# Kernel optimization log

Measured on AMD Instinct MI355X. Metric: run time of the kernel, lower is better.

## Reference

```python
import math
import jax, jax.numpy as jnp
import numpy as np

B, T, D = 8, 2048, 256
N_TICKS, DT, P_MIN, P_MAX = 3, 1.0, 2.0, 4.0


def setup_inputs() -> dict:
    key = jax.random.key(0)
    ks = jax.random.split(key, 16)
    s = 1.0 / math.sqrt(D)
    w = lambda k: jax.random.normal(k, (D, D), jnp.float32) * s
    zb = jnp.zeros((D,), jnp.float32)
    return {
        "z": jax.random.normal(ks[0], (B, T, D), jnp.float32),
        "in_w": w(ks[1]), "in_b": zb,
        "ln_g": jnp.ones((D,), jnp.float32), "ln_b": zb,
        "q_w": w(ks[2]), "q_b": zb,
        "k_w": w(ks[3]), "k_b": zb,
        "v_w": w(ks[4]), "v_b": zb,
        "o_w": w(ks[5]), "o_b": zb,
        "log_tau": jnp.zeros((D,), jnp.float32),
        "p1_w": w(ks[6]), "p1_b": zb,
        "p2_w": w(ks[7]), "p2_b": zb,
    }


def _layernorm(x, g, b, eps=1e-5):
    mu = jnp.mean(x, axis=-1, keepdims=True)
    var = jnp.var(x, axis=-1, keepdims=True)
    return (x - mu) * jax.lax.rsqrt(var + eps) * g + b


def _lin(x, w, b):
    return x @ w.T + b


def reference(z, in_w, in_b, ln_g, ln_b, q_w, q_b, k_w, k_b, v_w, v_b,
              o_w, o_b, log_tau, p1_w, p1_b, p2_w, p2_b):
    tau = jnp.exp(log_tau)  # [d]
    inv_sqrt_d = 1.0 / math.sqrt(D)
    uniform = 1.0 / T
    pred_losses, eff_ps = [], []
    for _ in range(N_TICKS):
        h = _layernorm(_lin(z, in_w, in_b), ln_g, ln_b)
        Q, K, V = _lin(h, q_w, q_b), _lin(h, k_w, k_b), _lin(h, v_w, v_b)
        sim = jnp.einsum('btd,bsd->bts', Q, K) * inv_sqrt_d  # [B,T,T]
        attn = jax.nn.softmax(sim, axis=-1)
        row_max = jnp.max(attn, axis=-1)  # [B,T]
        conf = (jnp.mean(row_max, axis=-1) - uniform) / (1.0 - uniform + 1e-6)
        conf = jnp.clip(conf, 0.0, 1.0)  # [B]
        eff_p = P_MIN + (P_MAX - P_MIN) * conf
        eff_ps.append(jax.lax.stop_gradient(eff_p))
        attn_sharp = jax.nn.softmax(sim * eff_p[:, None, None], axis=-1)
        context = jnp.einsum('bts,bsd->btd', attn_sharp, V)
        target = _lin(context, o_w, o_b)
        z_pred = _lin(jax.nn.relu(_lin(z, p1_w, p1_b)), p2_w, p2_b)
        dz = (target - z) / (tau + 1e-6)
        z_next = z + DT * dz
        pred_losses.append(jnp.mean((z_pred - jax.lax.stop_gradient(z_next)) ** 2))
        z = z_next
    pred_loss_mean = jnp.mean(jnp.stack(pred_losses))
    eff_p_mean = jnp.mean(jnp.concatenate(eff_ps))
    return z, pred_loss_mean, eff_p_mean
```

## Files before the change

kernel.cpp:

```cpp
#include <hip/hip_runtime.h>
#include <math.h>

#define Bn 8
#define Tn 2048
#define Dn 256
#define NTICK 3
#define NROWS (Bn*Tn)
#define ABM 64
#define NBLKA (NROWS/ABM)
#define BS 64
#define GM 64
#define NBLKG (NROWS/GM)
#define WP 65536

typedef unsigned int u32;
typedef unsigned short u16;
typedef __attribute__((ext_vector_type(8))) short bf16x8;
typedef __attribute__((ext_vector_type(4))) float f32x4;
typedef __attribute__((ext_vector_type(16))) float f32x16;

__device__ __forceinline__ float bf2f(u32 u){
  union { u32 i; float f; } x; x.i = u << 16; return x.f;
}
__device__ __forceinline__ u16 f2bf(float f){
  union { float f; u32 i; } x; x.f = f;
  u32 r = (x.i + 0x7fffu + ((x.i >> 16) & 1u)) >> 16;
  return (u16)r;
}
__device__ __forceinline__ void gld_lds16(const u16* gsrc, u16* ldst){
  __builtin_amdgcn_global_load_lds(
      (const __attribute__((address_space(1))) u32*)(const void*)gsrc,
      (__attribute__((address_space(3))) u32*)(void*)ldst, 16, 0, 0);
}

__device__ __forceinline__ void stage_A(const u16* __restrict__ A, int row0, char* smem){
  const int tid = threadIdx.x, lane = tid & 63, w = tid >> 6;
  #pragma unroll
  for (int r=0;r<8;++r){
    int s = w*16 + 2*r + (lane>>5);
    int slot = (lane & 31) ^ (s & 7);
    gld_lds16(A + (size_t)(row0 + s)*Dn + slot*8, (u16*)(smem + (w*16 + 2*r)*512));
  }
}
__device__ __forceinline__ void load_frags(const char* smem, bf16x8* af){
  const int tid = threadIdx.x, lane = tid & 63, w = tid >> 6;
  const int l7 = lane & 7, g = (lane >> 4) & 3, q15 = lane & 15;
  const char* ab = smem + (w*16 + q15)*512;
  #pragma unroll
  for (int kk=0;kk<8;++kk) af[kk] = *(const bf16x8*)(ab + 16*((4*kk+g)^l7));
}
__device__ __forceinline__ void stage_Wchunk(const u16* __restrict__ W, int c, char* wbuf){
  const int tid = threadIdx.x, lane = tid & 63, w = tid >> 6;
  #pragma unroll
  for (int r=0;r<2;++r){
    int rl = w*4 + 2*r + (lane>>5);
    int slot = (lane & 31) ^ (rl & 7);
    gld_lds16(W + (size_t)(c*16 + rl)*Dn + slot*8, (u16*)(wbuf + (w*4 + 2*r)*512));
  }
}
__device__ __forceinline__ void load_wfrags(const char* wbuf, bf16x8* wf){
  const int lane = threadIdx.x & 63;
  const int l7 = lane & 7, g = (lane >> 4) & 3, q15 = lane & 15;
  const char* wb_ = wbuf + q15*512;
  #pragma unroll
  for (int kk=0;kk<8;++kk) wf[kk] = *(const bf16x8*)(wb_ + 16*((4*kk+g)^l7));
}
__device__ __forceinline__ void zero_acc(f32x4* acc){
  #pragma unroll
  for (int nt=0;nt<16;++nt) acc[nt] = (f32x4){0.f,0.f,0.f,0.f};
}
#define CHUNK_STEP(c, NC, PLANE_OF, IDX_OF)                                    \
  asm volatile("s_waitcnt lgkmcnt(0)" ::: "memory");                           \
  if ((c) < (NC)-2) { asm volatile("s_waitcnt vmcnt(2)" ::: "memory"); }       \
  else              { asm volatile("s_waitcnt vmcnt(0)" ::: "memory"); }       \
  __builtin_amdgcn_sched_barrier(0);                                           \
  __builtin_amdgcn_s_barrier();                                                \
  if ((c)+3 < (NC)) stage_Wchunk(PLANE_OF((c)+3), IDX_OF((c)+3), ring + (((c)+3)&3)*8192);

__global__ void k_prep(const float* __restrict__ s0, const float* __restrict__ s1,
                       const float* __restrict__ s2, const float* __restrict__ s3,
                       const float* __restrict__ s4, const float* __restrict__ s5,
                       const float* __restrict__ s6, u16* __restrict__ dst){
  int y = blockIdx.y;
  const float* s = (y==0)?s0:(y==1)?s1:(y==2)?s2:(y==3)?s3:(y==4)?s4:(y==5)?s5:s6;
  int i = (blockIdx.x*256 + threadIdx.x)*4;
  float4 v = *(const float4*)(s + i);
  u16 h0=f2bf(v.x), h1=f2bf(v.y), h2=f2bf(v.z), h3=f2bf(v.w);
  uint2 hi, lo;
  hi.x = (u32)h0 | ((u32)h1 << 16);
  hi.y = (u32)h2 | ((u32)h3 << 16);
  lo.x = (u32)f2bf(v.x - bf2f(h0)) | ((u32)f2bf(v.y - bf2f(h1)) << 16);
  lo.y = (u32)f2bf(v.z - bf2f(h2)) | ((u32)f2bf(v.w - bf2f(h3)) << 16);
  *(uint2*)(dst + (size_t)y*WP + i) = hi;
  *(uint2*)(dst + (size_t)(7+y)*WP + i) = lo;
}

__global__ void k_split(const float* __restrict__ s, u16* __restrict__ dh, u16* __restrict__ dl,
                        float* __restrict__ stats){
  if (blockIdx.x == 0 && threadIdx.x < 64) stats[threadIdx.x] = 0.f;
  int i = (blockIdx.x*256 + threadIdx.x)*4;
  float4 v = *(const float4*)(s + i);
  u16 h0=f2bf(v.x), h1=f2bf(v.y), h2=f2bf(v.z), h3=f2bf(v.w);
  uint2 hi, lo;
  hi.x = (u32)h0 | ((u32)h1 << 16);
  hi.y = (u32)h2 | ((u32)h3 << 16);
  lo.x = (u32)f2bf(v.x - bf2f(h0)) | ((u32)f2bf(v.y - bf2f(h1)) << 16);
  lo.y = (u32)f2bf(v.z - bf2f(h2)) | ((u32)f2bf(v.w - bf2f(h3)) << 16);
  *(uint2*)(dh + i) = hi;
  *(uint2*)(dl + i) = lo;
}

__global__ __launch_bounds__(256) void k_gemm_ln(
    const u16* __restrict__ Ahi, const u16* __restrict__ Alo,
    const u16* __restrict__ Whi, const u16* __restrict__ Wlo,
    const float* __restrict__ bias, const float* __restrict__ gamma, const float* __restrict__ beta,
    u16* __restrict__ h)
{
  __shared__ __align__(16) char smem[65536];
  char* ring = smem;
  f32x4 acc[16];
  const int row0 = blockIdx.x * GM;
  stage_A(Ahi, row0, smem);
  stage_A(Alo, row0, smem + 32768);
  asm volatile("s_waitcnt vmcnt(0)" ::: "memory");
  __builtin_amdgcn_sched_barrier(0);
  bf16x8 afh[8], afl[8];
  load_frags(smem, afh);
  load_frags(smem + 32768, afl);
  asm volatile("s_waitcnt lgkmcnt(0)" ::: "memory");
  __builtin_amdgcn_sched_barrier(0);
  __builtin_amdgcn_s_barrier();
  zero_acc(acc);
  #define LN_PL(i) ((i) < 16 ? Whi : Wlo)
  #define LN_IX(i) ((i) & 15)
  stage_Wchunk(LN_PL(0), LN_IX(0), ring + 0*8192);
  stage_Wchunk(LN_PL(1), LN_IX(1), ring + 1*8192);
  stage_Wchunk(LN_PL(2), LN_IX(2), ring + 2*8192);
  asm volatile("s_waitcnt vmcnt(4)" ::: "memory");
  __builtin_amdgcn_sched_barrier(0);
  __builtin_amdgcn_s_barrier();
  for (int c=0; c<32; ++c){
    bf16x8 wf[8];
    load_wfrags(ring + (c&3)*8192, wf);
    int nt = c & 15;
    if (c < 16){
      #pragma unroll
      for (int kk=0;kk<8;++kk)
        acc[nt] = __builtin_amdgcn_mfma_f32_16x16x32_bf16(afh[kk], wf[kk], acc[nt], 0,0,0);
      #pragma unroll
      for (int kk=0;kk<8;++kk)
        acc[nt] = __builtin_amdgcn_mfma_f32_16x16x32_bf16(afl[kk], wf[kk], acc[nt], 0,0,0);
    } else {
      #pragma unroll
      for (int kk=0;kk<8;++kk)
        acc[nt] = __builtin_amdgcn_mfma_f32_16x16x32_bf16(afh[kk], wf[kk], acc[nt], 0,0,0);
    }
    CHUNK_STEP(c, 32, LN_PL, LN_IX)
  }
  const int tid = threadIdx.x, lane = tid & 63, w = tid >> 6;
  const int g4 = lane >> 4, q15 = lane & 15;
  float bcol[16], gcol[16], becol[16];
  #pragma unroll
  for (int nt=0;nt<16;++nt){
    int col = nt*16 + q15;
    bcol[nt] = bias[col]; gcol[nt] = gamma[col]; becol[nt] = beta[col];
  }
  float mu[4], rstd[4];
  #pragma unroll
  for (int j=0;j<4;++j){
    float s=0.f, q=0.f;
    #pragma unroll
    for (int nt=0;nt<16;++nt){ float v = acc[nt][j] + bcol[nt]; s += v; q += v*v; }
    #pragma unroll
    for (int off=1; off<16; off<<=1){ s += __shfl_xor(s,off); q += __shfl_xor(q,off); }
    float m = s*(1.f/Dn);
    mu[j] = m; rstd[j] = rsqrtf(q*(1.f/Dn) - m*m + 1e-5f);
  }
  const size_t rbase = (size_t)(row0 + w*16 + g4*4);
  #pragma unroll
  for (int nt=0;nt<16;++nt){
    #pragma unroll
    for (int j=0;j<4;++j){
      float v = (acc[nt][j] + bcol[nt] - mu[j])*rstd[j]*gcol[nt] + becol[nt];
      h[(rbase+j)*Dn + nt*16 + q15] = f2bf(v);
    }
  }
}

__global__ __launch_bounds__(256) void k_gemm_qkv(
    const u16* __restrict__ h, const u16* __restrict__ wbf,
    const float* __restrict__ qb, const float* __restrict__ kb, const float* __restrict__ vb,
    u16* __restrict__ Qo, u16* __restrict__ Ko, u16* __restrict__ Vo)
{
  __shared__ __align__(16) char smem[65536];
  char* ring = smem + 32768;
  f32x4 acc[16];
  const int row0 = blockIdx.x * GM;
  stage_A(h, row0, smem);
  #define QKV_PL(i) (wbf + ((size_t)((((i)>>5)+1) + (((i)>>4)&1)*7))*WP)
  #define QKV_IX(i) ((i) & 15)
  stage_Wchunk(QKV_PL(0), QKV_IX(0), ring + 0*8192);
  stage_Wchunk(QKV_PL(1), QKV_IX(1), ring + 1*8192);
  stage_Wchunk(QKV_PL(2), QKV_IX(2), ring + 2*8192);
  asm volatile("s_waitcnt vmcnt(4)" ::: "memory");
  __builtin_amdgcn_sched_barrier(0);
  bf16x8 af[8];
  load_frags(smem, af);
  zero_acc(acc);
  const int tid = threadIdx.x, lane = tid & 63, w = tid >> 6;
  const int g4 = lane >> 4, q15 = lane & 15;
  const size_t rbase = (size_t)(row0 + w*16 + g4*4);
  __builtin_amdgcn_s_barrier();
  for (int c=0; c<96; ++c){
    bf16x8 wf[8];
    load_wfrags(ring + (c&3)*8192, wf);
    int nt = c & 15;
    #pragma unroll
    for (int kk=0;kk<8;++kk)
      acc[nt] = __builtin_amdgcn_mfma_f32_16x16x32_bf16(af[kk], wf[kk], acc[nt], 0,0,0);
    CHUNK_STEP(c, 96, QKV_PL, QKV_IX)
    if ((c & 31) == 31){
      int p = c >> 5;
      const float* bias = (p==0) ? qb : (p==1) ? kb : vb;
      u16* out = (p==0) ? Qo : (p==1) ? Ko : Vo;
      #pragma unroll
      for (int nt2=0;nt2<16;++nt2){
        float bc = bias[nt2*16 + q15];
        #pragma unroll
        for (int j=0;j<4;++j)
          out[(rbase+j)*Dn + nt2*16 + q15] = f2bf(acc[nt2][j] + bc);
      }
      zero_acc(acc);
    }
  }
}

__global__ __launch_bounds__(256) void k_gemm_update(
    const u16* __restrict__ Chi, const u16* __restrict__ Clo,
    const u16* __restrict__ Whi, const u16* __restrict__ Wlo,
    const float* __restrict__ ob,
    const u16* __restrict__ zhi_old, const u16* __restrict__ zlo_old,
    const float* __restrict__ log_tau,
    u16* __restrict__ zhi_new, u16* __restrict__ zlo_new,
    float* __restrict__ zout)
{
  __shared__ __align__(16) char smem[65536];
  char* ring = smem;
  f32x4 acc[16];
  const int row0 = blockIdx.x * GM;
  stage_A(Chi, row0, smem);
  stage_A(Clo, row0, smem + 32768);
  asm volatile("s_waitcnt vmcnt(0)" ::: "memory");
  __builtin_amdgcn_sched_barrier(0);
  bf16x8 afh[8], afl[8];
  load_frags(smem, afh);
  load_frags(smem + 32768, afl);
  asm volatile("s_waitcnt lgkmcnt(0)" ::: "memory");
  __builtin_amdgcn_sched_barrier(0);
  __builtin_amdgcn_s_barrier();
  zero_acc(acc);
  stage_Wchunk(LN_PL(0), LN_IX(0), ring + 0*8192);
  stage_Wchunk(LN_PL(1), LN_IX(1), ring + 1*8192);
  stage_Wchunk(LN_PL(2), LN_IX(2), ring + 2*8192);
  asm volatile("s_waitcnt vmcnt(4)" ::: "memory");
  __builtin_amdgcn_sched_barrier(0);
  __builtin_amdgcn_s_barrier();
  for (int c=0; c<32; ++c){
    bf16x8 wf[8];
    load_wfrags(ring + (c&3)*8192, wf);
    int nt = c & 15;
    if (c < 16){
      #pragma unroll
      for (int kk=0;kk<8;++kk)
        acc[nt] = __builtin_amdgcn_mfma_f32_16x16x32_bf16(afh[kk], wf[kk], acc[nt], 0,0,0);
      #pragma unroll
      for (int kk=0;kk<8;++kk)
        acc[nt] = __builtin_amdgcn_mfma_f32_16x16x32_bf16(afl[kk], wf[kk], acc[nt], 0,0,0);
    } else {
      #pragma unroll
      for (int kk=0;kk<8;++kk)
        acc[nt] = __builtin_amdgcn_mfma_f32_16x16x32_bf16(afh[kk], wf[kk], acc[nt], 0,0,0);
    }
    CHUNK_STEP(c, 32, LN_PL, LN_IX)
  }
  const int tid = threadIdx.x, lane = tid & 63, w = tid >> 6;
  const int g4 = lane >> 4, q15 = lane & 15;
  const size_t rbase = (size_t)(row0 + w*16 + g4*4);
  #pragma unroll
  for (int nt=0;nt<16;++nt){
    int col = nt*16 + q15;
    float bc = ob[col];
    float invt = 1.f/(expf(log_tau[col]) + 1e-6f);
    #pragma unroll
    for (int j=0;j<4;++j){
      size_t idx = (rbase+j)*Dn + col;
      float zo = bf2f(zhi_old[idx]) + bf2f(zlo_old[idx]);
      float zn = zo + (acc[nt][j] + bc - zo)*invt;
      u16 zh = f2bf(zn);
      zhi_new[idx] = zh;
      zlo_new[idx] = f2bf(zn - bf2f(zh));
      if (zout) zout[idx] = zn;
    }
  }
}

__global__ __launch_bounds__(256) void k_gemm_relu(
    const u16* __restrict__ A, const u16* __restrict__ Wb, const float* __restrict__ bias,
    u16* __restrict__ t1)
{
  __shared__ __align__(16) char smem[65536];
  char* ring = smem + 32768;
  f32x4 acc[16];
  const int row0 = blockIdx.x * GM;
  stage_A(A, row0, smem);
  #define W1_PL(i) (Wb)
  #define W1_IX(i) (i)
  stage_Wchunk(Wb, 0, ring + 0*8192);
  stage_Wchunk(Wb, 1, ring + 1*8192);
  stage_Wchunk(Wb, 2, ring + 2*8192);
  asm volatile("s_waitcnt vmcnt(4)" ::: "memory");
  __builtin_amdgcn_sched_barrier(0);
  bf16x8 af[8];
  load_frags(smem, af);
  zero_acc(acc);
  __builtin_amdgcn_s_barrier();
  for (int c=0; c<16; ++c){
    bf16x8 wf[8];
    load_wfrags(ring + (c&3)*8192, wf);
    #pragma unroll
    for (int kk=0;kk<8;++kk)
      acc[c] = __builtin_amdgcn_mfma_f32_16x16x32_bf16(af[kk], wf[kk], acc[c], 0,0,0);
    CHUNK_STEP(c, 16, W1_PL, W1_IX)
  }
  const int tid = threadIdx.x, lane = tid & 63, w = tid >> 6;
  const int g4 = lane >> 4, q15 = lane & 15;
  const size_t rbase = (size_t)(row0 + w*16 + g4*4);
  #pragma unroll
  for (int nt=0;nt<16;++nt){
    float bc = bias[nt*16 + q15];
    #pragma unroll
    for (int j=0;j<4;++j)
      t1[(rbase+j)*Dn + nt*16 + q15] = f2bf(fmaxf(acc[nt][j] + bc, 0.f));
  }
}

__global__ __launch_bounds__(256) void k_gemm_loss(
    const u16* __restrict__ t1, const u16* __restrict__ Wb, const float* __restrict__ bias,
    const u16* __restrict__ zhi_new, const u16* __restrict__ zlo_new,
    float* __restrict__ loss_acc)
{
  __shared__ __align__(16) char smem[65536];
  __shared__ float red[4];
  char* ring = smem + 32768;
  f32x4 acc[16];
  const int row0 = blockIdx.x * GM;
  stage_A(t1, row0, smem);
  stage_Wchunk(Wb, 0, ring + 0*8192);
  stage_Wchunk(Wb, 1, ring + 1*8192);
  stage_Wchunk(Wb, 2, ring + 2*8192);
  asm volatile("s_waitcnt vmcnt(4)" ::: "memory");
  __builtin_amdgcn_sched_barrier(0);
  bf16x8 af[8];
  load_frags(smem, af);
  zero_acc(acc);
  __builtin_amdgcn_s_barrier();
  for (int c=0; c<16; ++c){
    bf16x8 wf[8];
    load_wfrags(ring + (c&3)*8192, wf);
    #pragma unroll
    for (int kk=0;kk<8;++kk)
      acc[c] = __builtin_amdgcn_mfma_f32_16x16x32_bf16(af[kk], wf[kk], acc[c], 0,0,0);
    CHUNK_STEP(c, 16, W1_PL, W1_IX)
  }
  const int tid = threadIdx.x, lane = tid & 63, w = tid >> 6;
  const int g4 = lane >> 4, q15 = lane & 15;
  const size_t rbase = (size_t)(row0 + w*16 + g4*4);
  float lsum = 0.f;
  #pragma unroll
  for (int nt=0;nt<16;++nt){
    float bc = bias[nt*16 + q15];
    #pragma unroll
    for (int j=0;j<4;++j){
      size_t idx = (rbase+j)*Dn + nt*16 + q15;
      float zn = bf2f(zhi_new[idx]) + bf2f(zlo_new[idx]);
      float dn = acc[nt][j] + bc - zn;
      lsum += dn*dn;
    }
  }
  #pragma unroll
  for (int off=1; off<64; off<<=1) lsum += __shfl_xor(lsum, off);
  if (lane == 0) red[w] = lsum;
  __syncthreads();
  if (tid == 0) atomicAdd(loss_acc, red[0]+red[1]+red[2]+red[3]);
}

__global__ __launch_bounds__(256) void k_passA(
    const u16* __restrict__ Qg, const u16* __restrict__ Kg,
    float* __restrict__ conf_b)
{
  __shared__ __align__(16) char smem[65536];
  const int tid = threadIdx.x;
  const int lane = tid & 63, w = tid >> 6;
  const int l31 = lane & 31, hi5 = lane >> 5;
  const int qh = w >> 1, sh = w & 1;
  const int row0 = blockIdx.x * ABM;
  const int b = row0 >> 11;
  const size_t kbase = (size_t)b * Tn * Dn;

  #pragma unroll
  for (int r=0;r<8;++r){
    int s = w*16 + 2*r + (lane>>5);
    int slot = (lane & 31) ^ (s & 7);
    gld_lds16(Qg + (size_t)(row0 + s)*Dn + slot*8, (u16*)(smem + (w*16 + 2*r)*512));
  }
  asm volatile("s_waitcnt vmcnt(0)" ::: "memory");
  __builtin_amdgcn_sched_barrier(0);
  __builtin_amdgcn_s_barrier();
  bf16x8 qf[16];
  {
    const char* qb = smem + (qh*32 + l31)*512;
    const int r7 = l31 & 7;
    #pragma unroll
    for (int t=0;t<16;++t) qf[t] = *(const bf16x8*)(qb + 16*((2*t+hi5)^r7));
  }
  asm volatile("s_waitcnt lgkmcnt(0)" ::: "memory");
  __builtin_amdgcn_sched_barrier(0);
  __builtin_amdgcn_s_barrier();
  #pragma unroll
  for (int r=0;r<8;++r){
    int s = w*16 + 2*r + (lane>>5);
    int slot = (lane & 31) ^ (s & 7);
    gld_lds16(Kg + kbase + (size_t)(s)*Dn + slot*8, (u16*)(smem + 32768 + (w*16 + 2*r)*512));
  }
  #pragma unroll
  for (int r=0;r<8;++r){
    int s = w*16 + 2*r + (lane>>5);
    int slot = (lane & 31) ^ (s & 7);
    gld_lds16(Kg + kbase + (size_t)(BS + s)*Dn + slot*8, (u16*)(smem + (w*16 + 2*r)*512));
  }
  asm volatile("s_waitcnt vmcnt(8)" ::: "memory");
  __builtin_amdgcn_sched_barrier(0);
  __builtin_amdgcn_s_barrier();

  float m_run = -INFINITY, l_run = 0.f;
  const int sr7 = l31 & 7;
  int cur = 1;
  for (int tile=0; tile<Tn/BS; ++tile){
    const char* kb = smem + cur*32768 + (sh*32 + l31)*512;
    f32x16 sc = (f32x16)(0.f);
    #pragma unroll
    for (int t=0;t<16;++t){
      bf16x8 kf = *(const bf16x8*)(kb + 16*((2*t+hi5)^sr7));
      sc = __builtin_amdgcn_mfma_f32_32x32x16_bf16(kf, qf[t], sc, 0,0,0);
    }
    float vmax = -INFINITY;
    float vals[16];
    #pragma unroll
    for (int i=0;i<16;++i){ float v = sc[i]*0.0625f; vals[i]=v; vmax=fmaxf(vmax,v); }
    vmax = fmaxf(vmax, __shfl_xor(vmax,32));
    float mnew = fmaxf(m_run, vmax);
    float corr = __expf(m_run - mnew);
    float esum = 0.f;
    #pragma unroll
    for (int i=0;i<16;++i) esum += __expf(vals[i]-mnew);
    esum += __shfl_xor(esum,32);
    l_run = l_run*corr + esum;
    m_run = mnew;

    asm volatile("s_waitcnt vmcnt(0)" ::: "memory");
    __builtin_amdgcn_sched_barrier(0);
    __builtin_amdgcn_s_barrier();
    if (tile < Tn/BS - 2){
      #pragma unroll
      for (int r=0;r<8;++r){
        int s = w*16 + 2*r + (lane>>5);
        int slot = (lane & 31) ^ (s & 7);
        gld_lds16(Kg + kbase + (size_t)((tile+2)*BS + s)*Dn + slot*8,
                  (u16*)(smem + cur*32768 + (w*16 + 2*r)*512));
      }
    }
    cur ^= 1;
  }
  __syncthreads();
  if (sh == 1 && lane < 32){
    float2 ml; ml.x = m_run; ml.y = l_run;
    *(float2*)(smem + (qh*32 + l31)*8) = ml;
  }
  __syncthreads();
  if (sh == 0){
    float2 o = *(const float2*)(smem + (qh*32 + l31)*8);
    float m2 = fmaxf(m_run, o.x);
    float lm = l_run*__expf(m_run - m2) + o.y*__expf(o.x - m2);
    float r1 = 1.f/lm;
    #pragma unroll
    for (int off=1; off<64; off<<=1) r1 += __shfl_xor(r1, off);
    if (lane==0) atomicAdd(conf_b + b, r1*0.5f);
  }
}

#define KB0 0
#define KB1 32768
#define VT0 65536
#define VT1 98304
#define PST 131072
__global__ __launch_bounds__(512) void k_passB(
    const u16* __restrict__ Qg, const u16* __restrict__ Kg, const u16* __restrict__ Vg,
    const float* __restrict__ conf_sum, u16* __restrict__ Chi, u16* __restrict__ Clo)
{
  __shared__ __align__(16) char smem[139264];
  const int tid = threadIdx.x;
  const int lane = tid & 63, w = tid >> 6;
  const int qg = w & 3, hs = w >> 2;
  const int l7 = lane & 7, g = (lane >> 4) & 3, q15 = lane & 15;
  const int row0 = blockIdx.x * ABM;
  const int b = row0 >> 11;
  const size_t kbase = (size_t)b * Tn * Dn;
  float mean_rm = conf_sum[b] * (1.f/Tn);
  float uniform = 1.f/Tn;
  float conf = fminf(fmaxf((mean_rm - uniform)/(1.f - uniform + 1e-6f), 0.f), 1.f);
  const float scale = (2.f + 2.f*conf) * 0.0625f;
  const int tid2 = tid & 255;
  const int dblk = tid2 >> 3, sblk = tid2 & 7;
  uint4 vreg[8];
  const int NT = Tn/BS;

  if (hs == 0){
    #pragma unroll
    for (int r=0;r<8;++r){
      int s = w*16 + 2*r + (lane>>5);
      int slot = (lane & 31) ^ (s & 7);
      gld_lds16(Qg + (size_t)(row0 + s)*Dn + slot*8, (u16*)(smem + KB0 + (w*16 + 2*r)*512));
    }
  } else {
    const u16* vsrc = Vg + kbase + (size_t)(sblk*8)*Dn + dblk*8;
    #pragma unroll
    for (int si=0; si<8; ++si) vreg[si] = *(const uint4*)(vsrc + (size_t)si*Dn);
  }
  __syncthreads();
  bf16x8 qf[8];
  {
    const char* qb = smem + KB0 + (qg*16 + q15)*512;
    #pragma unroll
    for (int kk=0;kk<8;++kk) qf[kk] = *(const bf16x8*)(qb + 16*((4*kk+g)^l7));
  }
  __syncthreads();
  if (hs == 0){
    #pragma unroll
    for (int r=0;r<8;++r){
      int s = w*16 + 2*r + (lane>>5);
      int slot = (lane & 31) ^ (s & 7);
      gld_lds16(Kg + kbase + (size_t)(s)*Dn + slot*8, (u16*)(smem + KB0 + (w*16 + 2*r)*512));
    }
    #pragma unroll
    for (int r=0;r<8;++r){
      int s = w*16 + 2*r + (lane>>5);
      int slot = (lane & 31) ^ (s & 7);
      gld_lds16(Kg + kbase + (size_t)(BS + s)*Dn + slot*8, (u16*)(smem + KB1 + (w*16 + 2*r)*512));
    }
    asm volatile("s_waitcnt vmcnt(8)" ::: "memory");
    __builtin_amdgcn_sched_barrier(0);
  } else {
    const u32* rw = (const u32*)vreg;
    #pragma unroll
    for (int dl=0; dl<8; ++dl){
      int wi = dl >> 1;
      u32 sel = (dl & 1) ? 0x07060302u : 0x05040100u;
      uint4 o;
      o.x = __builtin_amdgcn_perm(rw[1*4+wi], rw[0*4+wi], sel);
      o.y = __builtin_amdgcn_perm(rw[3*4+wi], rw[2*4+wi], sel);
      o.z = __builtin_amdgcn_perm(rw[5*4+wi], rw[4*4+wi], sel);
      o.w = __builtin_amdgcn_perm(rw[7*4+wi], rw[6*4+wi], sel);
      int d = dblk*8 + dl;
      *(uint4*)(smem + VT0 + d*128 + 16*(sblk ^ dl)) = o;
    }
    asm volatile("s_waitcnt lgkmcnt(0)" ::: "memory");
    __builtin_amdgcn_sched_barrier(0);
  }
  __builtin_amdgcn_s_barrier();

  float m_run = -INFINITY, l_run = 0.f;
  f32x4 oa[16];
  #pragma unroll
  for (int md=0;md<16;++md) oa[md] = (f32x4){0.f,0.f,0.f,0.f};

  char* pbase = smem + PST + w*1024 + q15*64;
  const int psw = q15 & 3;

  int cur = 0;
  for (int tile=0; tile<NT; ++tile){
    const char* kbuf = smem + (cur ? KB1 : KB0);
    const char* vbuf = smem + (cur ? VT1 : VT0);
    char* vbuf_n = (char*)smem + (cur ? VT0 : VT1);
    if (hs == 1 && tile < NT-1){
      const u16* vsrc = Vg + kbase + (size_t)((tile+1)*BS + sblk*8)*Dn + dblk*8;
      #pragma unroll
      for (int si=0; si<8; ++si) vreg[si] = *(const uint4*)(vsrc + (size_t)si*Dn);
    }
    f32x4 sc[2];
    sc[0] = (f32x4){0.f,0.f,0.f,0.f};
    sc[1] = (f32x4){0.f,0.f,0.f,0.f};
    #pragma unroll
    for (int kk=0;kk<8;++kk){
      #pragma unroll
      for (int msl=0;msl<2;++msl){
        int msg = 2*hs + msl;
        bf16x8 kf = *(const bf16x8*)(kbuf + (msg*16+q15)*512 + 16*((4*kk+g)^l7));
        sc[msl] = __builtin_amdgcn_mfma_f32_16x16x32_bf16(kf, qf[kk], sc[msl], 0,0,0);
      }
    }
    float vmax = -INFINITY;
    float vals[8];
    #pragma unroll
    for (int msl=0;msl<2;++msl){
      #pragma unroll
      for (int j=0;j<4;++j){ float v = sc[msl][j]*scale; vals[msl*4+j]=v; vmax=fmaxf(vmax,v); }
    }
    vmax = fmaxf(vmax, __shfl_xor(vmax,16));
    vmax = fmaxf(vmax, __shfl_xor(vmax,32));
    float mnew = fmaxf(m_run, vmax);
    float corr = __expf(m_run - mnew);
    float esum = 0.f;
    #pragma unroll
    for (int t2=0;t2<8;++t2){ float p = __expf(vals[t2]-mnew); vals[t2]=p; esum += p; }
    esum += __shfl_xor(esum,16); esum += __shfl_xor(esum,32);
    l_run = l_run*corr + esum;
    m_run = mnew;
    #pragma unroll
    for (int md=0;md<16;++md) oa[md] *= corr;
    #pragma unroll
    for (int msl=0;msl<2;++msl){
      uint2 pw;
      pw.x = (u32)f2bf(vals[msl*4+0]) | ((u32)f2bf(vals[msl*4+1]) << 16);
      pw.y = (u32)f2bf(vals[msl*4+2]) | ((u32)f2bf(vals[msl*4+3]) << 16);
      int slot = (2*msl + (g>>1)) ^ psw;
      *(uint2*)(pbase + slot*16 + (g&1)*8) = pw;
    }
    asm volatile("s_waitcnt lgkmcnt(0)" ::: "memory");
    __builtin_amdgcn_sched_barrier(0);
    {
      bf16x8 pf = *(const bf16x8*)(pbase + ((g ^ psw)*16));
      #pragma unroll
      for (int md=0; md<16; ++md){
        bf16x8 vf = *(const bf16x8*)(vbuf + (md*16+q15)*128 + 16*((4*hs+g)^l7));
        oa[md] = __builtin_amdgcn_mfma_f32_16x16x32_bf16(vf, pf, oa[md], 0,0,0);
      }
    }
    if (hs == 1){
      if (tile < NT-1){
        asm volatile("s_waitcnt vmcnt(0)" ::: "memory");
        __builtin_amdgcn_sched_barrier(0);
        const u32* rw = (const u32*)vreg;
        #pragma unroll
        for (int dl=0; dl<8; ++dl){
          int wi = dl >> 1;
          u32 sel = (dl & 1) ? 0x07060302u : 0x05040100u;
          uint4 o;
          o.x = __builtin_amdgcn_perm(rw[1*4+wi], rw[0*4+wi], sel);
          o.y = __builtin_amdgcn_perm(rw[3*4+wi], rw[2*4+wi], sel);
          o.z = __builtin_amdgcn_perm(rw[5*4+wi], rw[4*4+wi], sel);
          o.w = __builtin_amdgcn_perm(rw[7*4+wi], rw[6*4+wi], sel);
          int d = dblk*8 + dl;
          *(uint4*)(vbuf_n + d*128 + 16*(sblk ^ dl)) = o;
        }
      }
      asm volatile("s_waitcnt lgkmcnt(0)" ::: "memory");
    } else {
      asm volatile("s_waitcnt vmcnt(0) lgkmcnt(0)" ::: "memory");
    }
    __builtin_amdgcn_sched_barrier(0);
    __builtin_amdgcn_s_barrier();
    if (hs == 0 && tile < NT-2){
      #pragma unroll
      for (int r=0;r<8;++r){
        int s = w*16 + 2*r + (lane>>5);
        int slot = (lane & 31) ^ (s & 7);
        gld_lds16(Kg + kbase + (size_t)((tile+2)*BS + s)*Dn + slot*8,
                  (u16*)(smem + (cur ? KB1 : KB0) + (w*16 + 2*r)*512));
      }
    }
    cur ^= 1;
  }
  __syncthreads();
  if (hs == 1){
    char* ob_ = smem + (qg*64 + lane)*256;
    #pragma unroll
    for (int md=0; md<16; ++md)
      *(f32x4*)(ob_ + (md ^ q15)*16) = oa[md];
    float2 ml; ml.x = m_run; ml.y = l_run;
    *(float2*)(smem + VT0 + (qg*64 + lane)*8) = ml;
  }
  __syncthreads();
  if (hs == 0){
    float2 ml = *(const float2*)(smem + VT0 + (qg*64 + lane)*8);
    float m = fmaxf(m_run, ml.x);
    float ca = __expf(m_run - m), cb = __expf(ml.x - m);
    float l = l_run*ca + ml.y*cb;
    float inv = 1.f / l;
    const char* ob_ = smem + (qg*64 + lane)*256;
    const size_t rr = (size_t)(row0 + qg*16 + q15)*Dn + g*4;
    #pragma unroll
    for (int md=0; md<16; ++md){
      f32x4 ob = *(const f32x4*)(ob_ + (md ^ q15)*16);
      float v0 = (oa[md][0]*ca + ob[0]*cb)*inv;
      float v1 = (oa[md][1]*ca + ob[1]*cb)*inv;
      float v2 = (oa[md][2]*ca + ob[2]*cb)*inv;
      float v3 = (oa[md][3]*ca + ob[3]*cb)*inv;
      uint2 hi, lo;
      u16 h0=f2bf(v0), h1=f2bf(v1), h2=f2bf(v2), h3=f2bf(v3);
      hi.x = (u32)h0 | ((u32)h1 << 16);
      hi.y = (u32)h2 | ((u32)h3 << 16);
      lo.x = (u32)f2bf(v0 - bf2f(h0)) | ((u32)f2bf(v1 - bf2f(h1)) << 16);
      lo.y = (u32)f2bf(v2 - bf2f(h2)) | ((u32)f2bf(v3 - bf2f(h3)) << 16);
      *(uint2*)(Chi + rr + md*16) = hi;
      *(uint2*)(Clo + rr + md*16) = lo;
    }
  }
}

__global__ void k_finalize(const float* __restrict__ loss3, const float* __restrict__ conf_sum,
                           float* __restrict__ out_scalars){
  if (threadIdx.x == 0){
    float ls = (loss3[0]+loss3[1]+loss3[2]) * (1.f/(3.f*NROWS*Dn));
    float es = 0.f;
    float uniform = 1.f/Tn;
    #pragma unroll
    for (int i=0;i<NTICK*Bn;++i){
      float mean_rm = conf_sum[i] * (1.f/Tn);
      float conf = fminf(fmaxf((mean_rm - uniform)/(1.f - uniform + 1e-6f), 0.f), 1.f);
      es += 2.f + 2.f*conf;
    }
    out_scalars[0] = ls;
    out_scalars[1] = es * (1.f/(NTICK*Bn));
  }
}

extern "C" void kernel_launch(void* const* d_in, const int* in_sizes, int n_in,
                              void* d_out, int out_size, void* d_ws, size_t ws_size,
                              hipStream_t stream) {
  (void)in_sizes; (void)n_in; (void)out_size; (void)ws_size;
  const float* z_in   = (const float*)d_in[0];
  const float* in_w   = (const float*)d_in[1];
  const float* in_b   = (const float*)d_in[2];
  const float* ln_g   = (const float*)d_in[3];
  const float* ln_b   = (const float*)d_in[4];
  const float* q_w    = (const float*)d_in[5];
  const float* q_b    = (const float*)d_in[6];
  const float* k_w    = (const float*)d_in[7];
  const float* k_b    = (const float*)d_in[8];
  const float* v_w    = (const float*)d_in[9];
  const float* v_b    = (const float*)d_in[10];
  const float* o_w    = (const float*)d_in[11];
  const float* o_b    = (const float*)d_in[12];
  const float* log_tau= (const float*)d_in[13];
  const float* p1_w   = (const float*)d_in[14];
  const float* p1_b   = (const float*)d_in[15];
  const float* p2_w   = (const float*)d_in[16];
  const float* p2_b   = (const float*)d_in[17];

  float* out = (float*)d_out;
  const size_t NE = (size_t)NROWS * Dn;

  u16*  zh0  = (u16*)d_ws;
  u16*  zl0  = zh0 + NE;
  u16*  zh1  = zl0 + NE;
  u16*  zl1  = zh1 + NE;
  u16*  hbuf = zl1 + NE;
  u16*  Qb   = hbuf + NE;
  u16*  Kb   = Qb + NE;
  u16*  Vb   = Kb + NE;
  u16*  Chi  = Vb + NE;
  u16*  Clo  = Chi + NE;
  u16*  t1b  = Clo + NE;
  u16*  wbf  = t1b + NE;
  float* stats = (float*)(wbf + 14*WP);
  float* conf_sum = stats;
  float* loss     = stats + 24;

  k_prep<<<dim3(64,7), 256, 0, stream>>>(in_w, q_w, k_w, v_w, o_w, p1_w, p2_w, wbf);
  k_split<<<4096, 256, 0, stream>>>(z_in, zh0, zl0, stats);

  u16* zh_list[2] = { zh0, zh1 };
  u16* zl_list[2] = { zl0, zl1 };

  for (int t = 0; t < NTICK; ++t){
    u16* zh_old = zh_list[t & 1];
    u16* zl_old = zl_list[t & 1];
    u16* zh_new = zh_list[(t+1) & 1];
    u16* zl_new = zl_list[(t+1) & 1];
    float* zout = (t == NTICK-1) ? out : nullptr;
    k_gemm_ln<<<NBLKG, 256, 0, stream>>>(zh_old, zl_old, wbf + 0*WP, wbf + 7*WP,
                                         in_b, ln_g, ln_b, hbuf);
    k_gemm_qkv<<<NBLKG, 256, 0, stream>>>(hbuf, wbf, q_b, k_b, v_b, Qb, Kb, Vb);
    k_passA<<<NBLKA, 256, 0, stream>>>(Qb, Kb, conf_sum + t*8);
    k_passB<<<NBLKA, 512, 0, stream>>>(Qb, Kb, Vb, conf_sum + t*8, Chi, Clo);
    k_gemm_update<<<NBLKG, 256, 0, stream>>>(Chi, Clo, wbf + 4*WP, wbf + 11*WP, o_b,
                                             zh_old, zl_old, log_tau, zh_new, zl_new, zout);
    k_gemm_relu<<<NBLKG, 256, 0, stream>>>(zh_old, wbf + 5*WP, p1_b, t1b);
    k_gemm_loss<<<NBLKG, 256, 0, stream>>>(t1b, wbf + 6*WP, p2_b, zh_new, zl_new, loss + t);
  }
  k_finalize<<<1, 64, 0, stream>>>(loss, conf_sum, out + NE);
}
```

Measured before the change: 893.7 us.

## Split QKV GEMM across grid y-dimension and pad V tile stride in passB

The fused QKV GEMM kernel is launched with a 3-wide grid y-dimension so each block computes only one of Q, K or V. This triples the block count and shortens each block's serial loop, at the cost of restaging the A tile three times. In passB, the transposed V tile gets a padded row stride and an extra XOR swizzle to reduce LDS bank conflicts on the MFMA operand reads. That swizzle raises shared memory use per block.

```diff
diff --git a/kernel.cpp b/kernel.cpp
--- a/kernel.cpp
+++ b/kernel.cpp
@@ -192,46 +192,44 @@
     const float* __restrict__ qb, const float* __restrict__ kb, const float* __restrict__ vb,
     u16* __restrict__ Qo, u16* __restrict__ Ko, u16* __restrict__ Vo)
 {
+  const u16 *Whi, *Wlo; const float* bias; u16* out;
+  if (blockIdx.y == 0){ Whi = wbf + 1*WP; Wlo = wbf + 8*WP;  bias = qb; out = Qo; }
+  else if (blockIdx.y == 1){ Whi = wbf + 2*WP; Wlo = wbf + 9*WP;  bias = kb; out = Ko; }
+  else { Whi = wbf + 3*WP; Wlo = wbf + 10*WP; bias = vb; out = Vo; }
   __shared__ __align__(16) char smem[65536];
   char* ring = smem + 32768;
   f32x4 acc[16];
   const int row0 = blockIdx.x * GM;
   stage_A(h, row0, smem);
-  #define QKV_PL(i) (wbf + ((size_t)((((i)>>5)+1) + (((i)>>4)&1)*7))*WP)
-  #define QKV_IX(i) ((i) & 15)
-  stage_Wchunk(QKV_PL(0), QKV_IX(0), ring + 0*8192);
-  stage_Wchunk(QKV_PL(1), QKV_IX(1), ring + 1*8192);
-  stage_Wchunk(QKV_PL(2), QKV_IX(2), ring + 2*8192);
+  #define QK_PL(i) ((i) < 16 ? Whi : Wlo)
+  #define QK_IX(i) ((i) & 15)
+  stage_Wchunk(QK_PL(0), QK_IX(0), ring + 0*8192);
+  stage_Wchunk(QK_PL(1), QK_IX(1), ring + 1*8192);
+  stage_Wchunk(QK_PL(2), QK_IX(2), ring + 2*8192);
   asm volatile("s_waitcnt vmcnt(4)" ::: "memory");
   __builtin_amdgcn_sched_barrier(0);
   bf16x8 af[8];
   load_frags(smem, af);
   zero_acc(acc);
+  __builtin_amdgcn_s_barrier();
+  for (int c=0; c<32; ++c){
+    bf16x8 wf[8];
+    load_wfrags(ring + (c&3)*8192, wf);
+    int nt = c & 15;
+    #pragma unroll
+    for (int kk=0;kk<8;++kk)
+      acc[nt] = __builtin_amdgcn_mfma_f32_16x16x32_bf16(af[kk], wf[kk], acc[nt], 0,0,0);
+    CHUNK_STEP(c, 32, QK_PL, QK_IX)
+  }
   const int tid = threadIdx.x, lane = tid & 63, w = tid >> 6;
   const int g4 = lane >> 4, q15 = lane & 15;
   const size_t rbase = (size_t)(row0 + w*16 + g4*4);
-  __builtin_amdgcn_s_barrier();
-  for (int c=0; c<96; ++c){
-    bf16x8 wf[8];
-    load_wfrags(ring + (c&3)*8192, wf);
-    int nt = c & 15;
-    #pragma unroll
-    for (int kk=0;kk<8;++kk)
-      acc[nt] = __builtin_amdgcn_mfma_f32_16x16x32_bf16(af[kk], wf[kk], acc[nt], 0,0,0);
-    CHUNK_STEP(c, 96, QKV_PL, QKV_IX)
-    if ((c & 31) == 31){
-      int p = c >> 5;
-      const float* bias = (p==0) ? qb : (p==1) ? kb : vb;
-      u16* out = (p==0) ? Qo : (p==1) ? Ko : Vo;
-      #pragma unroll
-      for (int nt2=0;nt2<16;++nt2){
-        float bc = bias[nt2*16 + q15];
-        #pragma unroll
-        for (int j=0;j<4;++j)
-          out[(rbase+j)*Dn + nt2*16 + q15] = f2bf(acc[nt2][j] + bc);
-      }
-      zero_acc(acc);
-    }
+  #pragma unroll
+  for (int nt=0;nt<16;++nt){
+    float bc = bias[nt*16 + q15];
+    #pragma unroll
+    for (int j=0;j<4;++j)
+      out[(rbase+j)*Dn + nt*16 + q15] = f2bf(acc[nt][j] + bc);
   }
 }
 
@@ -501,13 +499,14 @@
 #define KB0 0
 #define KB1 32768
 #define VT0 65536
-#define VT1 98304
-#define PST 131072
+#define VT1 106496
+#define PST 147456
+#define VSTR 160
 __global__ __launch_bounds__(512) void k_passB(
     const u16* __restrict__ Qg, const u16* __restrict__ Kg, const u16* __restrict__ Vg,
     const float* __restrict__ conf_sum, u16* __restrict__ Chi, u16* __restrict__ Clo)
 {
-  __shared__ __align__(16) char smem[139264];
+  __shared__ __align__(16) char smem[155648];
   const int tid = threadIdx.x;
   const int lane = tid & 63, w = tid >> 6;
   const int qg = w & 3, hs = w >> 2;
@@ -571,7 +570,7 @@
       o.z = __builtin_amdgcn_perm(rw[5*4+wi], rw[4*4+wi], sel);
       o.w = __builtin_amdgcn_perm(rw[7*4+wi], rw[6*4+wi], sel);
       int d = dblk*8 + dl;
-      *(uint4*)(smem + VT0 + d*128 + 16*(sblk ^ dl)) = o;
+      *(uint4*)(smem + VT0 + d*VSTR + 16*((sblk ^ dl ^ (dblk&7)))) = o;
     }
     asm volatile("s_waitcnt lgkmcnt(0)" ::: "memory");
     __builtin_amdgcn_sched_barrier(0);
@@ -585,6 +584,7 @@
 
   char* pbase = smem + PST + w*1024 + q15*64;
   const int psw = q15 & 3;
+  const int vb0 = q15 >> 3;
 
   int cur = 0;
   for (int tile=0; tile<NT; ++tile){
@@ -641,7 +641,8 @@
       bf16x8 pf = *(const bf16x8*)(pbase + ((g ^ psw)*16));
       #pragma unroll
       for (int md=0; md<16; ++md){
-        bf16x8 vf = *(const bf16x8*)(vbuf + (md*16+q15)*128 + 16*((4*hs+g)^l7));
+        int vslot = (4*hs+g) ^ l7 ^ (((2*md)&7) ^ vb0);
+        bf16x8 vf = *(const bf16x8*)(vbuf + (md*16+q15)*VSTR + 16*vslot);
         oa[md] = __builtin_amdgcn_mfma_f32_16x16x32_bf16(vf, pf, oa[md], 0,0,0);
       }
     }
@@ -660,7 +661,7 @@
           o.z = __builtin_amdgcn_perm(rw[5*4+wi], rw[4*4+wi], sel);
           o.w = __builtin_amdgcn_perm(rw[7*4+wi], rw[6*4+wi], sel);
           int d = dblk*8 + dl;
-          *(uint4*)(vbuf_n + d*128 + 16*(sblk ^ dl)) = o;
+          *(uint4*)(vbuf_n + d*VSTR + 16*((sblk ^ dl ^ (dblk&7)))) = o;
         }
       }
       asm volatile("s_waitcnt lgkmcnt(0)" ::: "memory");
@@ -790,7 +791,7 @@
     float* zout = (t == NTICK-1) ? out : nullptr;
     k_gemm_ln<<<NBLKG, 256, 0, stream>>>(zh_old, zl_old, wbf + 0*WP, wbf + 7*WP,
                                          in_b, ln_g, ln_b, hbuf);
-    k_gemm_qkv<<<NBLKG, 256, 0, stream>>>(hbuf, wbf, q_b, k_b, v_b, Qb, Kb, Vb);
+    k_gemm_qkv<<<dim3(NBLKG,3), 256, 0, stream>>>(hbuf, wbf, q_b, k_b, v_b, Qb, Kb, Vb);
     k_passA<<<NBLKA, 256, 0, stream>>>(Qb, Kb, conf_sum + t*8);
     k_passB<<<NBLKA, 512, 0, stream>>>(Qb, Kb, Vb, conf_sum + t*8, Chi, Clo);
     k_gemm_update<<<NBLKG, 256, 0, stream>>>(Chi, Clo, wbf + 4*WP, wbf + 11*WP, o_b,
```

Result: faster. 800.2 us (-10.5%).
